# Performance work log

Measured on AMD Instinct MI355X. Metric: run time of the kernel, lower is better.

## Reference

```python
import jax, jax.numpy as jnp
import numpy as np

G_NUMS = 30      # group_nums
G_SIZE = 100     # group_size (also neighborhood_size)
BETA = 1.0
EPS = 1e-9


def setup_inputs() -> dict:
    key = jax.random.key(0)
    pointclouds = jax.random.normal(key, (8, 131072, 3), dtype=jnp.float32)
    return {"pointclouds": pointclouds}


def _knn_gather(points, queries, k):
    """points [b,N,3], queries [b,G,3] -> k nearest points per query [b,G,k,3]."""
    # squared distances [b,G,N]
    d2 = (
        jnp.sum(queries * queries, axis=-1)[..., None]
        - 2.0 * jnp.einsum("bgd,bnd->bgn", queries, points)
        + jnp.sum(points * points, axis=-1)[:, None, :]
    )
    _, idx = jax.lax.top_k(-d2, k)                    # [b,G,k]
    nbrs = jax.vmap(lambda p, i: p[i])(points, idx)   # [b,G,k,3]
    return nbrs


def reference(pointclouds):
    b, N, _ = pointclouds.shape
    # --- group_points: uniform-stride sampled centers, k-NN groups, group means ---
    stride = N // G_NUMS
    centers = pointclouds[:, ::stride][:, :G_NUMS]                 # [b,G,3]
    grouped = _knn_gather(pointclouds, centers, G_SIZE)            # [b,G,K,3]
    group_means = jnp.mean(grouped, axis=2)                        # [b,G,3]

    # --- estimate_pointcloud_local_coord_frames: per-group 3x3 PCA ---
    nbrs = _knn_gather(pointclouds, group_means, G_SIZE)           # [b,G,K,3]
    mu = jnp.mean(nbrs, axis=2, keepdims=True)
    X = nbrs - mu
    cov = jnp.einsum("bgkd,bgke->bgde", X, X) / G_SIZE             # [b,G,3,3]
    curvatures, frames = jnp.linalg.eigh(cov)                      # eigvals ascending

    # --- elongated-shape loss ---
    denom = curvatures[..., 0] + curvatures[..., 1] + curvatures[..., 2] + EPS
    first_vec = curvatures[..., 2] / denom
    second_vec = curvatures[..., 1] / denom
    elongated_shape_loss = -jnp.sum(first_vec - second_vec) / b

    # --- angular smoothness cost over group means / principal directions ---
    dirs = frames[..., :, 2]                                       # [b,G,3] largest-eig direction
    dm = jnp.sum(
        (group_means[:, :, None, :] - group_means[:, None, :, :]) ** 2, axis=-1
    )                                                              # [b,G,G]
    dm = dm + jnp.eye(G_NUMS, dtype=dm.dtype) * jnp.float32(1e30)  # exclude self
    j = jnp.argmin(dm, axis=-1)                                    # [b,G]
    dirs_j = jnp.take_along_axis(dirs, j[..., None], axis=1)       # [b,G,3]
    cos = jnp.sum(dirs * dirs_j, axis=-1)
    dlo_smooth_loss = jnp.mean(1.0 - cos * cos)                    # sign-invariant angle cost

    return elongated_shape_loss + BETA * dlo_smooth_loss
```

## Files before the change

### kernel.cpp

```cpp
#include <hip/hip_runtime.h>
#include <math.h>

#define N_PTS     131072
#define G_NUMS    30
#define G_SIZE    100
#define PT_STRIDE (N_PTS / G_NUMS)
#define TPB       1024
#define NWAVES    (TPB / 64)
#define BINS      4096
#define JB        (BINS / TPB)
#define SHIFT     20
#define SAMPLE_GRPS 1024
#define RANK_CUT  32
#define CAP       3072
#define TIE_CAP   64

struct KSmem {
    union {
        unsigned hist[BINS];
        struct {
            float gm[256][3];
            float dir[256][3];
            float pe[NWAVES];
            float ps[NWAVES];
        } fin;
    };
    unsigned wsum[NWAVES];
    unsigned T;
    int ns, nd, nt;
    unsigned u[CAP];
    int idx[CAP];
    float px[CAP], py[CAP], pz[CAP];
    int sel[G_SIZE];
    unsigned tu[TIE_CAP];
    int ti[TIE_CAP];
    float acc[3], cov[6], q[3];
    unsigned tau0, maxu, r1;
    float delta2;
};

__device__ __forceinline__ float dist2f(float px, float py, float pz,
                                        float qx, float qy, float qz) {
    float dx = px - qx, dy = py - qy, dz = pz - qz;
    return fmaf(dx, dx, fmaf(dy, dy, dz * dz));
}

__device__ __forceinline__ unsigned find_bin(KSmem& sm, unsigned rank,
                                             int tid, int lane, int wid) {
    unsigned hv[JB], csum = 0;
#pragma unroll
    for (int j = 0; j < JB; j++) { hv[j] = sm.hist[tid * JB + j]; csum += hv[j]; }
    unsigned inc = csum;
#pragma unroll
    for (int off = 1; off < 64; off <<= 1) {
        unsigned n = __shfl_up(inc, off);
        if (lane >= off) inc += n;
    }
    __syncthreads();
    if (lane == 63) sm.wsum[wid] = inc;
    __syncthreads();
    unsigned base = 0;
    for (int w = 0; w < wid; w++) base += sm.wsum[w];
    unsigned c = base + inc - csum;
#pragma unroll
    for (int j = 0; j < JB; j++) {
        if (c < rank && c + hv[j] >= rank) sm.T = (unsigned)(tid * JB + j);
        c += hv[j];
    }
    __syncthreads();
    return sm.T;
}

__device__ __forceinline__ void push4(KSmem& sm, const float4& xv, const float4& yv,
                                      const float4& zv, int i, unsigned tau,
                                      float qx, float qy, float qz) {
    unsigned u0 = __float_as_uint(dist2f(xv.x, yv.x, zv.x, qx, qy, qz));
    unsigned u1 = __float_as_uint(dist2f(xv.y, yv.y, zv.y, qx, qy, qz));
    unsigned u2 = __float_as_uint(dist2f(xv.z, yv.z, zv.z, qx, qy, qz));
    unsigned u3 = __float_as_uint(dist2f(xv.w, yv.w, zv.w, qx, qy, qz));
    int i0 = i * 4;
    if (u0 < tau) { int p = atomicAdd(&sm.ns, 1); if (p < CAP) { sm.u[p] = u0; sm.idx[p] = i0;     sm.px[p] = xv.x; sm.py[p] = yv.x; sm.pz[p] = zv.x; } }
    if (u1 < tau) { int p = atomicAdd(&sm.ns, 1); if (p < CAP) { sm.u[p] = u1; sm.idx[p] = i0 + 1; sm.px[p] = xv.y; sm.py[p] = yv.y; sm.pz[p] = zv.y; } }
    if (u2 < tau) { int p = atomicAdd(&sm.ns, 1); if (p < CAP) { sm.u[p] = u2; sm.idx[p] = i0 + 2; sm.px[p] = xv.z; sm.py[p] = yv.z; sm.pz[p] = zv.z; } }
    if (u3 < tau) { int p = atomicAdd(&sm.ns, 1); if (p < CAP) { sm.u[p] = u3; sm.idx[p] = i0 + 3; sm.px[p] = xv.w; sm.py[p] = yv.w; sm.pz[p] = zv.w; } }
}

template<bool SOA>
__device__ void knn_select(const float4* __restrict__ P4,
                           const float4* __restrict__ X4,
                           const float4* __restrict__ Y4,
                           const float4* __restrict__ Z4,
                           KSmem& sm, float qx, float qy, float qz,
                           int tid, int lane, int wid, bool save_tau) {
    for (int j = tid; j < BINS; j += TPB) sm.hist[j] = 0u;
    if (tid == 0) { sm.ns = 0; sm.nd = 0; sm.nt = 0; sm.T = 0u; }
    __syncthreads();

    if constexpr (SOA) {
        for (int i = tid; i < SAMPLE_GRPS; i += TPB) {
            float4 xv = X4[i], yv = Y4[i], zv = Z4[i];
            atomicAdd(&sm.hist[__float_as_uint(dist2f(xv.x, yv.x, zv.x, qx, qy, qz)) >> SHIFT], 1u);
            atomicAdd(&sm.hist[__float_as_uint(dist2f(xv.y, yv.y, zv.y, qx, qy, qz)) >> SHIFT], 1u);
            atomicAdd(&sm.hist[__float_as_uint(dist2f(xv.z, yv.z, zv.z, qx, qy, qz)) >> SHIFT], 1u);
            atomicAdd(&sm.hist[__float_as_uint(dist2f(xv.w, yv.w, zv.w, qx, qy, qz)) >> SHIFT], 1u);
        }
    } else {
        for (int grp = tid; grp < SAMPLE_GRPS; grp += TPB) {
            float4 f0 = P4[3 * grp + 0];
            float4 f1 = P4[3 * grp + 1];
            float4 f2 = P4[3 * grp + 2];
            atomicAdd(&sm.hist[__float_as_uint(dist2f(f0.x, f0.y, f0.z, qx, qy, qz)) >> SHIFT], 1u);
            atomicAdd(&sm.hist[__float_as_uint(dist2f(f0.w, f1.x, f1.y, qx, qy, qz)) >> SHIFT], 1u);
            atomicAdd(&sm.hist[__float_as_uint(dist2f(f1.z, f1.w, f2.x, qx, qy, qz)) >> SHIFT], 1u);
            atomicAdd(&sm.hist[__float_as_uint(dist2f(f2.y, f2.z, f2.w, qx, qy, qz)) >> SHIFT], 1u);
        }
    }
    __syncthreads();
    unsigned Tc = find_bin(sm, RANK_CUT, tid, lane, wid);
    const unsigned tau = (Tc >= BINS - 1) ? 0xFFFFFFFFu : ((Tc + 1) << SHIFT);
    if (save_tau && tid == 0) sm.tau0 = tau;
    for (int j = tid; j < BINS; j += TPB) sm.hist[j] = 0u;
    __syncthreads();

    if constexpr (SOA) {
        for (int base = 0; base < N_PTS / 4; base += TPB * 4) {
            int ia = base + tid, ib = ia + TPB, ic = ib + TPB, id_ = ic + TPB;
            float4 xa = X4[ia], ya = Y4[ia], za = Z4[ia];
            float4 xb = X4[ib], yb = Y4[ib], zb = Z4[ib];
            float4 xc = X4[ic], yc = Y4[ic], zc = Z4[ic];
            float4 xd = X4[id_], yd = Y4[id_], zd = Z4[id_];
            push4(sm, xa, ya, za, ia, tau, qx, qy, qz);
            push4(sm, xb, yb, zb, ib, tau, qx, qy, qz);
            push4(sm, xc, yc, zc, ic, tau, qx, qy, qz);
            push4(sm, xd, yd, zd, id_, tau, qx, qy, qz);
        }
    } else {
#pragma unroll 4
        for (int grp = tid; grp < N_PTS / 4; grp += TPB) {
            float4 f0 = P4[3 * grp + 0];
            float4 f1 = P4[3 * grp + 1];
            float4 f2 = P4[3 * grp + 2];
            float4 xv = make_float4(f0.x, f0.w, f1.z, f2.y);
            float4 yv = make_float4(f0.y, f1.x, f1.w, f2.z);
            float4 zv = make_float4(f0.z, f1.y, f2.x, f2.w);
            push4(sm, xv, yv, zv, grp, tau, qx, qy, qz);
        }
    }
    __syncthreads();
    int S = sm.ns; if (S > CAP) S = CAP;

    unsigned hb = 32u - (unsigned)__clz(tau - 1u);
    unsigned s2 = hb > 12u ? hb - 12u : 0u;
    for (int i = tid; i < S; i += TPB) atomicAdd(&sm.hist[sm.u[i] >> s2], 1u);
    __syncthreads();
    unsigned T2 = find_bin(sm, G_SIZE, tid, lane, wid);
    const unsigned lo = T2 << s2;

    for (int i = tid; i < S; i += TPB) {
        unsigned uu = sm.u[i];
        if (uu < lo) {
            int p = atomicAdd(&sm.nd, 1);
            if (p < G_SIZE) sm.sel[p] = i;
        } else if ((uu >> s2) == T2) {
            int p = atomicAdd(&sm.nt, 1);
            if (p < TIE_CAP) { sm.tu[p] = uu; sm.ti[p] = i; }
        }
    }
    __syncthreads();
    if (tid == 0) {
        int nd = sm.nd; if (nd > G_SIZE) nd = G_SIZE;
        int need = G_SIZE - nd;
        int ec = sm.nt; if (ec > TIE_CAP) ec = TIE_CAP;
        for (int a = 0; a < need && a < ec; ++a) {
            int best = a;
            for (int j = a + 1; j < ec; ++j)
                if (sm.tu[j] < sm.tu[best] ||
                    (sm.tu[j] == sm.tu[best] && sm.idx[sm.ti[j]] < sm.idx[sm.ti[best]])) best = j;
            unsigned tub = sm.tu[best]; sm.tu[best] = sm.tu[a]; sm.tu[a] = tub;
            int tib = sm.ti[best]; sm.ti[best] = sm.ti[a]; sm.ti[a] = tib;
            sm.sel[nd + a] = sm.ti[a];
        }
    }
    __syncthreads();
}

__device__ void eig3(const float cf[6], double lam_out[3], double dir_out[3]) {
    double a[3][3], v[3][3];
    a[0][0] = cf[0]; a[0][1] = cf[1]; a[0][2] = cf[2];
    a[1][0] = cf[1]; a[1][1] = cf[3]; a[1][2] = cf[4];
    a[2][0] = cf[2]; a[2][1] = cf[4]; a[2][2] = cf[5];
    for (int i = 0; i < 3; i++)
        for (int j = 0; j < 3; j++) v[i][j] = (i == j) ? 1.0 : 0.0;

    for (int sweep = 0; sweep < 12; sweep++) {
        double off = a[0][1] * a[0][1] + a[0][2] * a[0][2] + a[1][2] * a[1][2];
        if (off == 0.0) break;
        for (int p = 0; p < 2; p++) {
            for (int q = p + 1; q < 3; q++) {
                double apq = a[p][q];
                if (apq == 0.0) continue;
                double app = a[p][p], aqq = a[q][q];
                double theta = (aqq - app) / (2.0 * apq);
                double t = (theta >= 0.0 ? 1.0 : -1.0) /
                           (fabs(theta) + sqrt(theta * theta + 1.0));
                double c = 1.0 / sqrt(t * t + 1.0);
                double s = t * c;
                a[p][p] = app - t * apq;
                a[q][q] = aqq + t * apq;
                a[p][q] = 0.0; a[q][p] = 0.0;
                for (int r = 0; r < 3; r++) {
                    if (r == p || r == q) continue;
                    double arp = a[r][p], arq = a[r][q];
                    a[r][p] = c * arp - s * arq; a[p][r] = a[r][p];
                    a[r][q] = s * arp + c * arq; a[q][r] = a[r][q];
                }
                for (int r = 0; r < 3; r++) {
                    double vrp = v[r][p], vrq = v[r][q];
                    v[r][p] = c * vrp - s * vrq;
                    v[r][q] = s * vrp + c * vrq;
                }
            }
        }
    }
    double l0 = a[0][0], l1 = a[1][1], l2 = a[2][2];
    int i0 = 0, i1 = 1, i2 = 2;
    if (l0 > l1) { double t = l0; l0 = l1; l1 = t; int ti = i0; i0 = i1; i1 = ti; }
    if (l1 > l2) { double t = l1; l1 = l2; l2 = t; int ti = i1; i1 = i2; i2 = ti; }
    if (l0 > l1) { double t = l0; l0 = l1; l1 = t; int ti = i0; i0 = i1; i1 = ti; }
    lam_out[0] = l0; lam_out[1] = l1; lam_out[2] = l2;
    dir_out[0] = v[0][i2]; dir_out[1] = v[1][i2]; dir_out[2] = v[2][i2];
}

template<bool SOA>
__global__ __launch_bounds__(TPB)
void fused_knn_kernel(const float* __restrict__ pts,
                      const float* __restrict__ sx, const float* __restrict__ sy,
                      const float* __restrict__ sz,
                      float* __restrict__ gmeans, float* __restrict__ covs,
                      float* __restrict__ out,
                      unsigned* __restrict__ syncw,
                      int B, int nblk) {
    __shared__ KSmem sm;
    __shared__ int s_fastok;
    __shared__ int s_last;

    const int blk = blockIdx.x;
    const int b = blk % B;
    const int g = blk / B;
    const int gi = b * G_NUMS + g;
    const float* __restrict__ P = pts + (size_t)b * (N_PTS * 3);
    const float4* __restrict__ P4 = (const float4*)P;
    const float4* X4 = nullptr; const float4* Y4 = nullptr; const float4* Z4 = nullptr;
    if constexpr (SOA) {
        X4 = (const float4*)(sx + (size_t)b * N_PTS);
        Y4 = (const float4*)(sy + (size_t)b * N_PTS);
        Z4 = (const float4*)(sz + (size_t)b * N_PTS);
    }
    const int tid = threadIdx.x;
    const int lane = tid & 63, wid = tid >> 6;

    if (tid == 0) {
        const float* qp = P + (size_t)g * PT_STRIDE * 3;
        sm.q[0] = qp[0]; sm.q[1] = qp[1]; sm.q[2] = qp[2];
    }
    if (tid < 3) sm.acc[tid] = 0.f;
    if (tid < 6) sm.cov[tid] = 0.f;
    __syncthreads();
    const float qx = sm.q[0], qy = sm.q[1], qz = sm.q[2];

    knn_select<SOA>(P4, X4, Y4, Z4, sm, qx, qy, qz, tid, lane, wid, true);

    if (tid < G_SIZE) {
        int p = sm.sel[tid];
        atomicAdd(&sm.acc[0], sm.px[p]);
        atomicAdd(&sm.acc[1], sm.py[p]);
        atomicAdd(&sm.acc[2], sm.pz[p]);
    }
    __syncthreads();
    const int S0 = sm.ns;
    if (tid == 0) {
        float mx = sm.acc[0] * (1.0f / G_SIZE);
        float my = sm.acc[1] * (1.0f / G_SIZE);
        float mz = sm.acc[2] * (1.0f / G_SIZE);
        gmeans[(size_t)gi * 3 + 0] = mx;
        gmeans[(size_t)gi * 3 + 1] = my;
        gmeans[(size_t)gi * 3 + 2] = mz;
        float dx = mx - qx, dy = my - qy, dz = mz - qz;
        sm.delta2 = fmaf(dx, dx, fmaf(dy, dy, dz * dz));
        sm.q[0] = mx; sm.q[1] = my; sm.q[2] = mz;
        sm.acc[0] = 0.f; sm.acc[1] = 0.f; sm.acc[2] = 0.f;
        sm.maxu = 0u; sm.r1 = 0u; sm.T = 0u;
        sm.nd = 0; sm.nt = 0;
        s_last = 0;
        s_fastok = 0;
    }
    __syncthreads();
    const float q1x = sm.q[0], q1y = sm.q[1], q1z = sm.q[2];

    const bool attempt = (S0 >= G_SIZE) && (S0 <= CAP);
    if (attempt) {
        for (int j = tid; j < BINS; j += TPB) sm.hist[j] = 0u;
        for (int i = tid; i < S0; i += TPB) {
            unsigned uu = __float_as_uint(
                dist2f(sm.px[i], sm.py[i], sm.pz[i], q1x, q1y, q1z));
            sm.u[i] = uu;
            atomicMax(&sm.maxu, uu);
        }
        __syncthreads();
        unsigned maxu = sm.maxu;
        unsigned hb = (maxu == 0u) ? 0u : (32u - (unsigned)__clz(maxu));
        unsigned s3 = hb > 12u ? hb - 12u : 0u;
        for (int i = tid; i < S0; i += TPB) atomicAdd(&sm.hist[sm.u[i] >> s3], 1u);
        __syncthreads();
        unsigned T2 = find_bin(sm, G_SIZE, tid, lane, wid);
        const unsigned lo = T2 << s3;
        for (int i = tid; i < S0; i += TPB) {
            unsigned uu = sm.u[i];
            if (uu < lo) {
                int p = atomicAdd(&sm.nd, 1);
                if (p < G_SIZE) sm.sel[p] = i;
            } else if ((uu >> s3) == T2) {
                int p = atomicAdd(&sm.nt, 1);
                if (p < TIE_CAP) { sm.tu[p] = uu; sm.ti[p] = i; }
            }
        }
        __syncthreads();
        if (tid == 0) {
            int ok = 1;
            int nd = sm.nd; if (nd > G_SIZE) { nd = G_SIZE; ok = 0; }
            int need = G_SIZE - nd;
            if (sm.nt > TIE_CAP) ok = 0;
            int ec = sm.nt; if (ec > TIE_CAP) ec = TIE_CAP;
            if (need > ec) ok = 0;
            for (int a = 0; a < need && a < ec; ++a) {
                int best = a;
                for (int j = a + 1; j < ec; ++j)
                    if (sm.tu[j] < sm.tu[best] ||
                        (sm.tu[j] == sm.tu[best] && sm.idx[sm.ti[j]] < sm.idx[sm.ti[best]])) best = j;
                unsigned tub = sm.tu[best]; sm.tu[best] = sm.tu[a]; sm.tu[a] = tub;
                int tib = sm.ti[best]; sm.ti[best] = sm.ti[a]; sm.ti[a] = tib;
                sm.sel[nd + a] = sm.ti[a];
            }
            s_fastok = ok;
        }
        __syncthreads();
        if (s_fastok) {
            if (tid < G_SIZE) atomicMax(&sm.r1, sm.u[sm.sel[tid]]);
            __syncthreads();
            if (tid == 0) {
                double R0 = sqrt((double)__uint_as_float(sm.tau0));
                double dl = sqrt((double)sm.delta2);
                double r1 = sqrt((double)__uint_as_float(sm.r1));
                if (!((R0 - dl) > r1 * 1.0001 + 1e-7)) s_fastok = 0;
            }
            __syncthreads();
        }
    }

    if (!attempt || !s_fastok) {
        knn_select<SOA>(P4, X4, Y4, Z4, sm, q1x, q1y, q1z, tid, lane, wid, false);
    }

    float px = 0.f, py = 0.f, pz = 0.f;
    if (tid < G_SIZE) {
        int p = sm.sel[tid];
        px = sm.px[p]; py = sm.py[p]; pz = sm.pz[p];
        atomicAdd(&sm.acc[0], px);
        atomicAdd(&sm.acc[1], py);
        atomicAdd(&sm.acc[2], pz);
    }
    __syncthreads();
    float mx = sm.acc[0] * (1.0f / G_SIZE);
    float my = sm.acc[1] * (1.0f / G_SIZE);
    float mz = sm.acc[2] * (1.0f / G_SIZE);
    if (tid < G_SIZE) {
        float x = px - mx, y = py - my, z = pz - mz;
        atomicAdd(&sm.cov[0], x * x);
        atomicAdd(&sm.cov[1], x * y);
        atomicAdd(&sm.cov[2], x * z);
        atomicAdd(&sm.cov[3], y * y);
        atomicAdd(&sm.cov[4], y * z);
        atomicAdd(&sm.cov[5], z * z);
    }
    __syncthreads();
    if (tid < 6) covs[(size_t)gi * 6 + tid] = sm.cov[tid] * (1.0f / G_SIZE);

    __syncthreads();
    if (tid == 0) {
        unsigned old = __hip_atomic_fetch_add(&syncw[0], 1u, __ATOMIC_RELEASE,
                                              __HIP_MEMORY_SCOPE_AGENT);
        s_last = (old == (unsigned)(nblk - 1)) ? 1 : 0;
    }
    __syncthreads();
    if (!s_last) return;

    (void)__hip_atomic_load(&syncw[0], __ATOMIC_ACQUIRE, __HIP_MEMORY_SCOPE_AGENT);
    const int NG = nblk;
    float et = 0.f;
    if (tid < NG) {
        float cf[6];
#pragma unroll
        for (int j = 0; j < 6; j++) cf[j] = covs[tid * 6 + j];
        double lam[3], dir[3];
        eig3(cf, lam, dir);
        double denom = lam[0] + lam[1] + lam[2] + 1e-9;
        et = (float)((lam[2] - lam[1]) / denom);
        sm.fin.dir[tid][0] = (float)dir[0];
        sm.fin.dir[tid][1] = (float)dir[1];
        sm.fin.dir[tid][2] = (float)dir[2];
        sm.fin.gm[tid][0] = gmeans[tid * 3 + 0];
        sm.fin.gm[tid][1] = gmeans[tid * 3 + 1];
        sm.fin.gm[tid][2] = gmeans[tid * 3 + 2];
    }
    __syncthreads();

    float st = 0.f;
    if (tid < NG) {
        int bb = tid / G_NUMS, gg0 = tid % G_NUMS;
        float gx = sm.fin.gm[tid][0], gy = sm.fin.gm[tid][1], gz = sm.fin.gm[tid][2];
        float bd = 3.4e38f; int bj = 0;
        for (int gg = 0; gg < G_NUMS; gg++) {
            if (gg == gg0) continue;
            int o = bb * G_NUMS + gg;
            float dx = gx - sm.fin.gm[o][0];
            float dy = gy - sm.fin.gm[o][1];
            float dz = gz - sm.fin.gm[o][2];
            float d = dx * dx + dy * dy + dz * dz;
            if (d < bd) { bd = d; bj = gg; }
        }
        int o = bb * G_NUMS + bj;
        float cosv = sm.fin.dir[tid][0] * sm.fin.dir[o][0] +
                     sm.fin.dir[tid][1] * sm.fin.dir[o][1] +
                     sm.fin.dir[tid][2] * sm.fin.dir[o][2];
        st = 1.f - cosv * cosv;
    }

    float e = et, s2 = st;
#pragma unroll
    for (int off = 32; off > 0; off >>= 1) {
        e += __shfl_down(e, off);
        s2 += __shfl_down(s2, off);
    }
    if (lane == 0) { sm.fin.pe[wid] = e; sm.fin.ps[wid] = s2; }
    __syncthreads();
    if (tid == 0) {
        float se = 0.f, ss = 0.f;
        for (int w = 0; w < NWAVES; w++) { se += sm.fin.pe[w]; ss += sm.fin.ps[w]; }
        out[0] = -se / (float)B + ss / (float)NG;
    }
}

__global__ __launch_bounds__(256)
void transpose_kernel(const float* __restrict__ pts,
                      float* __restrict__ sx, float* __restrict__ sy,
                      float* __restrict__ sz, int total4) {
    int t = blockIdx.x * 256 + threadIdx.x;
    if (t >= total4) return;
    const float4* __restrict__ P4 = (const float4*)pts;
    float4 f0 = P4[3 * t + 0];
    float4 f1 = P4[3 * t + 1];
    float4 f2 = P4[3 * t + 2];
    ((float4*)sx)[t] = make_float4(f0.x, f0.w, f1.z, f2.y);
    ((float4*)sy)[t] = make_float4(f0.y, f1.x, f1.w, f2.z);
    ((float4*)sz)[t] = make_float4(f0.z, f1.y, f2.x, f2.w);
}

extern "C" void kernel_launch(void* const* d_in, const int* in_sizes, int n_in,
                              void* d_out, int out_size, void* d_ws, size_t ws_size,
                              hipStream_t stream) {
    const float* pts = (const float*)d_in[0];
    float* out = (float*)d_out;
    float* ws = (float*)d_ws;
    int B = in_sizes[0] / (N_PTS * 3);
    int nblk = B * G_NUMS;

    float* gmeans = ws;
    float* covs = ws + (size_t)B * G_NUMS * 3;
    const size_t base_floats = (size_t)B * G_NUMS * 9;
    unsigned* syncw = (unsigned*)(ws + base_floats);
    float* soa = ws + base_floats + 16;
    const size_t soa_floats = 3 * (size_t)B * N_PTS;
    const bool use_soa = ws_size >= (base_floats + 16 + soa_floats) * sizeof(float);

    hipMemsetAsync(syncw, 0, 64, stream);

    dim3 grid(nblk);
    if (use_soa) {
        float* sx = soa;
        float* sy = sx + (size_t)B * N_PTS;
        float* sz = sy + (size_t)B * N_PTS;
        int total4 = B * N_PTS / 4;
        transpose_kernel<<<dim3((total4 + 255) / 256), dim3(256), 0, stream>>>(
            pts, sx, sy, sz, total4);
        fused_knn_kernel<true><<<grid, TPB, 0, stream>>>(
            pts, sx, sy, sz, gmeans, covs, out, syncw, B, nblk);
    } else {
        fused_knn_kernel<false><<<grid, TPB, 0, stream>>>(
            pts, nullptr, nullptr, nullptr, gmeans, covs, out, syncw, B, nblk);
    }
}
```

Baseline: 140.1 us.

## Replace SoA float transpose with 8-bit quantized coordinate planes for KNN prefilter

```diff
diff --git a/kernel.cpp b/kernel.cpp
--- a/kernel.cpp
+++ b/kernel.cpp
@@ -14,6 +14,11 @@
 #define RANK_CUT  32
 #define CAP       3072
 #define TIE_CAP   64
+#define QS        0.0625f
+#define QOFF      (-8.0f + 0.03125f)
+#define QMARGIN   0.0542f
+
+typedef unsigned char uchar_t;
 
 struct KSmem {
     union {
@@ -71,6 +76,45 @@
     return sm.T;
 }
 
+__device__ void fine_select(KSmem& sm, unsigned ubound, int tid, int lane, int wid) {
+    int S = sm.ns; if (S > CAP) S = CAP;
+    unsigned hb = 32u - (unsigned)__clz(ubound | 1u);
+    unsigned s2 = hb > 12u ? hb - 12u : 0u;
+    for (int i = tid; i < S; i += TPB) {
+        unsigned bin = sm.u[i] >> s2; if (bin > BINS - 1u) bin = BINS - 1u;
+        atomicAdd(&sm.hist[bin], 1u);
+    }
+    __syncthreads();
+    unsigned T2 = find_bin(sm, G_SIZE, tid, lane, wid);
+    for (int i = tid; i < S; i += TPB) {
+        unsigned uu = sm.u[i];
+        unsigned bin = uu >> s2; if (bin > BINS - 1u) bin = BINS - 1u;
+        if (bin < T2) {
+            int p = atomicAdd(&sm.nd, 1);
+            if (p < G_SIZE) sm.sel[p] = i;
+        } else if (bin == T2) {
+            int p = atomicAdd(&sm.nt, 1);
+            if (p < TIE_CAP) { sm.tu[p] = uu; sm.ti[p] = i; }
+        }
+    }
+    __syncthreads();
+    if (tid == 0) {
+        int nd = sm.nd; if (nd > G_SIZE) nd = G_SIZE;
+        int need = G_SIZE - nd;
+        int ec = sm.nt; if (ec > TIE_CAP) ec = TIE_CAP;
+        for (int a = 0; a < need && a < ec; ++a) {
+            int best = a;
+            for (int j = a + 1; j < ec; ++j)
+                if (sm.tu[j] < sm.tu[best] ||
+                    (sm.tu[j] == sm.tu[best] && sm.idx[sm.ti[j]] < sm.idx[sm.ti[best]])) best = j;
+            unsigned tub = sm.tu[best]; sm.tu[best] = sm.tu[a]; sm.tu[a] = tub;
+            int tib = sm.ti[best]; sm.ti[best] = sm.ti[a]; sm.ti[a] = tib;
+            sm.sel[nd + a] = sm.ti[a];
+        }
+    }
+    __syncthreads();
+}
+
 __device__ __forceinline__ void push4(KSmem& sm, const float4& xv, const float4& yv,
                                       const float4& zv, int i, unsigned tau,
                                       float qx, float qy, float qz) {
@@ -85,103 +129,113 @@
     if (u3 < tau) { int p = atomicAdd(&sm.ns, 1); if (p < CAP) { sm.u[p] = u3; sm.idx[p] = i0 + 3; sm.px[p] = xv.w; sm.py[p] = yv.w; sm.pz[p] = zv.w; } }
 }
 
-template<bool SOA>
-__device__ void knn_select(const float4* __restrict__ P4,
-                           const float4* __restrict__ X4,
-                           const float4* __restrict__ Y4,
-                           const float4* __restrict__ Z4,
-                           KSmem& sm, float qx, float qy, float qz,
-                           int tid, int lane, int wid, bool save_tau) {
+__device__ void filter_exact(const float4* __restrict__ P4, KSmem& sm, unsigned tau,
+                             float qx, float qy, float qz, int tid) {
+    if (tid == 0) sm.ns = 0;
+    __syncthreads();
+#pragma unroll 4
+    for (int grp = tid; grp < N_PTS / 4; grp += TPB) {
+        float4 f0 = P4[3 * grp + 0];
+        float4 f1 = P4[3 * grp + 1];
+        float4 f2 = P4[3 * grp + 2];
+        float4 xv = make_float4(f0.x, f0.w, f1.z, f2.y);
+        float4 yv = make_float4(f0.y, f1.x, f1.w, f2.z);
+        float4 zv = make_float4(f0.z, f1.y, f2.x, f2.w);
+        push4(sm, xv, yv, zv, grp, tau, qx, qy, qz);
+    }
+    __syncthreads();
+}
+
+__device__ unsigned sample_tau(const float4* __restrict__ P4, KSmem& sm,
+                               float qx, float qy, float qz,
+                               int tid, int lane, int wid) {
     for (int j = tid; j < BINS; j += TPB) sm.hist[j] = 0u;
     if (tid == 0) { sm.ns = 0; sm.nd = 0; sm.nt = 0; sm.T = 0u; }
     __syncthreads();
-
-    if constexpr (SOA) {
-        for (int i = tid; i < SAMPLE_GRPS; i += TPB) {
-            float4 xv = X4[i], yv = Y4[i], zv = Z4[i];
-            atomicAdd(&sm.hist[__float_as_uint(dist2f(xv.x, yv.x, zv.x, qx, qy, qz)) >> SHIFT], 1u);
-            atomicAdd(&sm.hist[__float_as_uint(dist2f(xv.y, yv.y, zv.y, qx, qy, qz)) >> SHIFT], 1u);
-            atomicAdd(&sm.hist[__float_as_uint(dist2f(xv.z, yv.z, zv.z, qx, qy, qz)) >> SHIFT], 1u);
-            atomicAdd(&sm.hist[__float_as_uint(dist2f(xv.w, yv.w, zv.w, qx, qy, qz)) >> SHIFT], 1u);
-        }
-    } else {
-        for (int grp = tid; grp < SAMPLE_GRPS; grp += TPB) {
-            float4 f0 = P4[3 * grp + 0];
-            float4 f1 = P4[3 * grp + 1];
-            float4 f2 = P4[3 * grp + 2];
-            atomicAdd(&sm.hist[__float_as_uint(dist2f(f0.x, f0.y, f0.z, qx, qy, qz)) >> SHIFT], 1u);
-            atomicAdd(&sm.hist[__float_as_uint(dist2f(f0.w, f1.x, f1.y, qx, qy, qz)) >> SHIFT], 1u);
-            atomicAdd(&sm.hist[__float_as_uint(dist2f(f1.z, f1.w, f2.x, qx, qy, qz)) >> SHIFT], 1u);
-            atomicAdd(&sm.hist[__float_as_uint(dist2f(f2.y, f2.z, f2.w, qx, qy, qz)) >> SHIFT], 1u);
-        }
+    for (int grp = tid; grp < SAMPLE_GRPS; grp += TPB) {
+        float4 f0 = P4[3 * grp + 0];
+        float4 f1 = P4[3 * grp + 1];
+        float4 f2 = P4[3 * grp + 2];
+        atomicAdd(&sm.hist[__float_as_uint(dist2f(f0.x, f0.y, f0.z, qx, qy, qz)) >> SHIFT], 1u);
+        atomicAdd(&sm.hist[__float_as_uint(dist2f(f0.w, f1.x, f1.y, qx, qy, qz)) >> SHIFT], 1u);
+        atomicAdd(&sm.hist[__float_as_uint(dist2f(f1.z, f1.w, f2.x, qx, qy, qz)) >> SHIFT], 1u);
+        atomicAdd(&sm.hist[__float_as_uint(dist2f(f2.y, f2.z, f2.w, qx, qy, qz)) >> SHIFT], 1u);
     }
     __syncthreads();
     unsigned Tc = find_bin(sm, RANK_CUT, tid, lane, wid);
-    const unsigned tau = (Tc >= BINS - 1) ? 0xFFFFFFFFu : ((Tc + 1) << SHIFT);
+    unsigned tau = (Tc >= BINS - 1) ? 0xFFFFFFFFu : ((Tc + 1) << SHIFT);
+    for (int j = tid; j < BINS; j += TPB) sm.hist[j] = 0u;
+    __syncthreads();
+    return tau;
+}
+
+__device__ void knn_exact(const float4* __restrict__ P4, KSmem& sm,
+                          float qx, float qy, float qz,
+                          int tid, int lane, int wid, bool save_tau) {
+    unsigned tau = sample_tau(P4, sm, qx, qy, qz, tid, lane, wid);
     if (save_tau && tid == 0) sm.tau0 = tau;
-    for (int j = tid; j < BINS; j += TPB) sm.hist[j] = 0u;
-    __syncthreads();
-
-    if constexpr (SOA) {
-        for (int base = 0; base < N_PTS / 4; base += TPB * 4) {
-            int ia = base + tid, ib = ia + TPB, ic = ib + TPB, id_ = ic + TPB;
-            float4 xa = X4[ia], ya = Y4[ia], za = Z4[ia];
-            float4 xb = X4[ib], yb = Y4[ib], zb = Z4[ib];
-            float4 xc = X4[ic], yc = Y4[ic], zc = Z4[ic];
-            float4 xd = X4[id_], yd = Y4[id_], zd = Z4[id_];
-            push4(sm, xa, ya, za, ia, tau, qx, qy, qz);
-            push4(sm, xb, yb, zb, ib, tau, qx, qy, qz);
-            push4(sm, xc, yc, zc, ic, tau, qx, qy, qz);
-            push4(sm, xd, yd, zd, id_, tau, qx, qy, qz);
-        }
-    } else {
-#pragma unroll 4
-        for (int grp = tid; grp < N_PTS / 4; grp += TPB) {
-            float4 f0 = P4[3 * grp + 0];
-            float4 f1 = P4[3 * grp + 1];
-            float4 f2 = P4[3 * grp + 2];
-            float4 xv = make_float4(f0.x, f0.w, f1.z, f2.y);
-            float4 yv = make_float4(f0.y, f1.x, f1.w, f2.z);
-            float4 zv = make_float4(f0.z, f1.y, f2.x, f2.w);
-            push4(sm, xv, yv, zv, grp, tau, qx, qy, qz);
-        }
-    }
-    __syncthreads();
-    int S = sm.ns; if (S > CAP) S = CAP;
-
-    unsigned hb = 32u - (unsigned)__clz(tau - 1u);
-    unsigned s2 = hb > 12u ? hb - 12u : 0u;
-    for (int i = tid; i < S; i += TPB) atomicAdd(&sm.hist[sm.u[i] >> s2], 1u);
-    __syncthreads();
-    unsigned T2 = find_bin(sm, G_SIZE, tid, lane, wid);
-    const unsigned lo = T2 << s2;
-
+    filter_exact(P4, sm, tau, qx, qy, qz, tid);
+    fine_select(sm, tau, tid, lane, wid);
+}
+
+__device__ __forceinline__ void q8filt4(KSmem& sm, unsigned xw, unsigned yw,
+                                        unsigned zw, int i0, float tauf,
+                                        float Cx, float Cy, float Cz) {
+#pragma unroll
+    for (int j = 0; j < 4; ++j) {
+        float dx = fmaf((float)((xw >> (8 * j)) & 0xffu), QS, Cx);
+        float dy = fmaf((float)((yw >> (8 * j)) & 0xffu), QS, Cy);
+        float dz = fmaf((float)((zw >> (8 * j)) & 0xffu), QS, Cz);
+        float d2 = fmaf(dx, dx, fmaf(dy, dy, dz * dz));
+        if (d2 < tauf) {
+            int p = atomicAdd(&sm.ns, 1);
+            if (p < CAP) sm.idx[p] = i0 + j;
+        }
+    }
+}
+
+__device__ void knn_q8(const float* __restrict__ P, const float4* __restrict__ P4,
+                       const uint4* __restrict__ XQ, const uint4* __restrict__ YQ,
+                       const uint4* __restrict__ ZQ, KSmem& sm,
+                       float qx, float qy, float qz, int tid, int lane, int wid) {
+    unsigned tau = sample_tau(P4, sm, qx, qy, qz, tid, lane, wid);
+    if (tid == 0) { sm.tau0 = tau; sm.ns = 0; }
+    __syncthreads();
+    const bool bad_tau = (tau >= 0x7F800000u);
+    float tauf = 0.f; unsigned umax = 0u;
+    if (!bad_tau) {
+        float rt = sqrtf(__uint_as_float(tau)) + QMARGIN;
+        tauf = rt * rt;
+        float rm = sqrtf(tauf) + QMARGIN;
+        umax = __float_as_uint(fmaf(rm, rm, 1e-6f) * 1.0001f);
+
+        const float Cx = QOFF - qx, Cy = QOFF - qy, Cz = QOFF - qz;
+#pragma unroll 2
+        for (int it = 0; it < N_PTS / 16 / TPB; ++it) {
+            int i = it * TPB + tid;
+            uint4 xv = XQ[i], yv = YQ[i], zv = ZQ[i];
+            int i0 = i * 16;
+            q8filt4(sm, xv.x, yv.x, zv.x, i0 + 0,  tauf, Cx, Cy, Cz);
+            q8filt4(sm, xv.y, yv.y, zv.y, i0 + 4,  tauf, Cx, Cy, Cz);
+            q8filt4(sm, xv.z, yv.z, zv.z, i0 + 8,  tauf, Cx, Cy, Cz);
+            q8filt4(sm, xv.w, yv.w, zv.w, i0 + 12, tauf, Cx, Cy, Cz);
+        }
+        __syncthreads();
+    }
+    int S = sm.ns;
+    if (bad_tau || S > CAP) {
+        filter_exact(P4, sm, tau, qx, qy, qz, tid);
+        fine_select(sm, tau, tid, lane, wid);
+        return;
+    }
     for (int i = tid; i < S; i += TPB) {
-        unsigned uu = sm.u[i];
-        if (uu < lo) {
-            int p = atomicAdd(&sm.nd, 1);
-            if (p < G_SIZE) sm.sel[p] = i;
-        } else if ((uu >> s2) == T2) {
-            int p = atomicAdd(&sm.nt, 1);
-            if (p < TIE_CAP) { sm.tu[p] = uu; sm.ti[p] = i; }
-        }
-    }
-    __syncthreads();
-    if (tid == 0) {
-        int nd = sm.nd; if (nd > G_SIZE) nd = G_SIZE;
-        int need = G_SIZE - nd;
-        int ec = sm.nt; if (ec > TIE_CAP) ec = TIE_CAP;
-        for (int a = 0; a < need && a < ec; ++a) {
-            int best = a;
-            for (int j = a + 1; j < ec; ++j)
-                if (sm.tu[j] < sm.tu[best] ||
-                    (sm.tu[j] == sm.tu[best] && sm.idx[sm.ti[j]] < sm.idx[sm.ti[best]])) best = j;
-            unsigned tub = sm.tu[best]; sm.tu[best] = sm.tu[a]; sm.tu[a] = tub;
-            int tib = sm.ti[best]; sm.ti[best] = sm.ti[a]; sm.ti[a] = tib;
-            sm.sel[nd + a] = sm.ti[a];
-        }
-    }
-    __syncthreads();
+        const float* pp = P + 3 * (size_t)sm.idx[i];
+        float x = pp[0], y = pp[1], z = pp[2];
+        sm.px[i] = x; sm.py[i] = y; sm.pz[i] = z;
+        sm.u[i] = __float_as_uint(dist2f(x, y, z, qx, qy, qz));
+    }
+    __syncthreads();
+    fine_select(sm, umax, tid, lane, wid);
 }
 
 __device__ void eig3(const float cf[6], double lam_out[3], double dir_out[3]) {
@@ -191,7 +245,6 @@
     a[2][0] = cf[2]; a[2][1] = cf[4]; a[2][2] = cf[5];
     for (int i = 0; i < 3; i++)
         for (int j = 0; j < 3; j++) v[i][j] = (i == j) ? 1.0 : 0.0;
-
     for (int sweep = 0; sweep < 12; sweep++) {
         double off = a[0][1] * a[0][1] + a[0][2] * a[0][2] + a[1][2] * a[1][2];
         if (off == 0.0) break;
@@ -231,11 +284,11 @@
     dir_out[0] = v[0][i2]; dir_out[1] = v[1][i2]; dir_out[2] = v[2][i2];
 }
 
-template<bool SOA>
+template<int MODE>
 __global__ __launch_bounds__(TPB)
 void fused_knn_kernel(const float* __restrict__ pts,
-                      const float* __restrict__ sx, const float* __restrict__ sy,
-                      const float* __restrict__ sz,
+                      const uchar_t* __restrict__ xq, const uchar_t* __restrict__ yq,
+                      const uchar_t* __restrict__ zq,
                       float* __restrict__ gmeans, float* __restrict__ covs,
                       float* __restrict__ out,
                       unsigned* __restrict__ syncw,
@@ -243,6 +296,7 @@
     __shared__ KSmem sm;
     __shared__ int s_fastok;
     __shared__ int s_last;
+    __shared__ int s_exact;
 
     const int blk = blockIdx.x;
     const int b = blk % B;
@@ -250,11 +304,11 @@
     const int gi = b * G_NUMS + g;
     const float* __restrict__ P = pts + (size_t)b * (N_PTS * 3);
     const float4* __restrict__ P4 = (const float4*)P;
-    const float4* X4 = nullptr; const float4* Y4 = nullptr; const float4* Z4 = nullptr;
-    if constexpr (SOA) {
-        X4 = (const float4*)(sx + (size_t)b * N_PTS);
-        Y4 = (const float4*)(sy + (size_t)b * N_PTS);
-        Z4 = (const float4*)(sz + (size_t)b * N_PTS);
+    const uint4* XQ = nullptr; const uint4* YQ = nullptr; const uint4* ZQ = nullptr;
+    if (MODE == 1) {
+        XQ = (const uint4*)(xq + (size_t)b * N_PTS);
+        YQ = (const uint4*)(yq + (size_t)b * N_PTS);
+        ZQ = (const uint4*)(zq + (size_t)b * N_PTS);
     }
     const int tid = threadIdx.x;
     const int lane = tid & 63, wid = tid >> 6;
@@ -262,13 +316,15 @@
     if (tid == 0) {
         const float* qp = P + (size_t)g * PT_STRIDE * 3;
         sm.q[0] = qp[0]; sm.q[1] = qp[1]; sm.q[2] = qp[2];
+        s_exact = (MODE == 0) ? 1 : (syncw[1] ? 1 : 0);
     }
     if (tid < 3) sm.acc[tid] = 0.f;
     if (tid < 6) sm.cov[tid] = 0.f;
     __syncthreads();
     const float qx = sm.q[0], qy = sm.q[1], qz = sm.q[2];
 
-    knn_select<SOA>(P4, X4, Y4, Z4, sm, qx, qy, qz, tid, lane, wid, true);
+    if (s_exact) knn_exact(P4, sm, qx, qy, qz, tid, lane, wid, true);
+    else         knn_q8(P, P4, XQ, YQ, ZQ, sm, qx, qy, qz, tid, lane, wid);
 
     if (tid < G_SIZE) {
         int p = sm.sel[tid];
@@ -358,7 +414,7 @@
     }
 
     if (!attempt || !s_fastok) {
-        knn_select<SOA>(P4, X4, Y4, Z4, sm, q1x, q1y, q1z, tid, lane, wid, false);
+        knn_exact(P4, sm, q1x, q1y, q1z, tid, lane, wid, false);
     }
 
     float px = 0.f, py = 0.f, pz = 0.f;
@@ -435,13 +491,13 @@
         st = 1.f - cosv * cosv;
     }
 
-    float e = et, s2 = st;
+    float e = et, s2v = st;
 #pragma unroll
     for (int off = 32; off > 0; off >>= 1) {
         e += __shfl_down(e, off);
-        s2 += __shfl_down(s2, off);
-    }
-    if (lane == 0) { sm.fin.pe[wid] = e; sm.fin.ps[wid] = s2; }
+        s2v += __shfl_down(s2v, off);
+    }
+    if (lane == 0) { sm.fin.pe[wid] = e; sm.fin.ps[wid] = s2v; }
     __syncthreads();
     if (tid == 0) {
         float se = 0.f, ss = 0.f;
@@ -451,18 +507,37 @@
 }
 
 __global__ __launch_bounds__(256)
-void transpose_kernel(const float* __restrict__ pts,
-                      float* __restrict__ sx, float* __restrict__ sy,
-                      float* __restrict__ sz, int total4) {
+void quant_kernel(const float* __restrict__ pts,
+                  uchar_t* __restrict__ xq, uchar_t* __restrict__ yq,
+                  uchar_t* __restrict__ zq, unsigned* __restrict__ syncw,
+                  int total4) {
     int t = blockIdx.x * 256 + threadIdx.x;
     if (t >= total4) return;
     const float4* __restrict__ P4 = (const float4*)pts;
     float4 f0 = P4[3 * t + 0];
     float4 f1 = P4[3 * t + 1];
     float4 f2 = P4[3 * t + 2];
-    ((float4*)sx)[t] = make_float4(f0.x, f0.w, f1.z, f2.y);
-    ((float4*)sy)[t] = make_float4(f0.y, f1.x, f1.w, f2.z);
-    ((float4*)sz)[t] = make_float4(f0.z, f1.y, f2.x, f2.w);
+    float xs[4] = {f0.x, f0.w, f1.z, f2.y};
+    float ys[4] = {f0.y, f1.x, f1.w, f2.z};
+    float zs[4] = {f0.z, f1.y, f2.x, f2.w};
+    unsigned xb = 0, yb = 0, zb = 0; int bad = 0;
+#pragma unroll
+    for (int j = 0; j < 4; ++j) {
+        int ix = (int)floorf((xs[j] + 8.0f) * 16.0f);
+        int iy = (int)floorf((ys[j] + 8.0f) * 16.0f);
+        int iz = (int)floorf((zs[j] + 8.0f) * 16.0f);
+        if ((unsigned)ix > 255u || (unsigned)iy > 255u || (unsigned)iz > 255u) bad = 1;
+        ix = ix < 0 ? 0 : (ix > 255 ? 255 : ix);
+        iy = iy < 0 ? 0 : (iy > 255 ? 255 : iy);
+        iz = iz < 0 ? 0 : (iz > 255 ? 255 : iz);
+        xb |= (unsigned)ix << (8 * j);
+        yb |= (unsigned)iy << (8 * j);
+        zb |= (unsigned)iz << (8 * j);
+    }
+    ((unsigned*)xq)[t] = xb;
+    ((unsigned*)yq)[t] = yb;
+    ((unsigned*)zq)[t] = zb;
+    if (bad) atomicOr(&syncw[1], 1u);
 }
 
 extern "C" void kernel_launch(void* const* d_in, const int* in_sizes, int n_in,
@@ -475,27 +550,28 @@
     int nblk = B * G_NUMS;
 
     float* gmeans = ws;
-    float* covs = ws + (size_t)B * G_NUMS * 3;
-    const size_t base_floats = (size_t)B * G_NUMS * 9;
-    unsigned* syncw = (unsigned*)(ws + base_floats);
-    float* soa = ws + base_floats + 16;
-    const size_t soa_floats = 3 * (size_t)B * N_PTS;
-    const bool use_soa = ws_size >= (base_floats + 16 + soa_floats) * sizeof(float);
+    float* covs = ws + (size_t)3 * nblk;
+    unsigned* syncw = (unsigned*)(ws + (size_t)9 * nblk);
+    size_t plane_off = ((size_t)9 * nblk + 16) * 4;
+    plane_off = (plane_off + 15) & ~(size_t)15;
+    uchar_t* xq = (uchar_t*)d_ws + plane_off;
+    size_t planeB = (size_t)B * N_PTS;
+    uchar_t* yq = xq + planeB;
+    uchar_t* zq = yq + planeB;
+    size_t need = plane_off + 3 * planeB;
+    const int use_q = ws_size >= need;
 
     hipMemsetAsync(syncw, 0, 64, stream);
 
     dim3 grid(nblk);
-    if (use_soa) {
-        float* sx = soa;
-        float* sy = sx + (size_t)B * N_PTS;
-        float* sz = sy + (size_t)B * N_PTS;
+    if (use_q) {
         int total4 = B * N_PTS / 4;
-        transpose_kernel<<<dim3((total4 + 255) / 256), dim3(256), 0, stream>>>(
-            pts, sx, sy, sz, total4);
-        fused_knn_kernel<true><<<grid, TPB, 0, stream>>>(
-            pts, sx, sy, sz, gmeans, covs, out, syncw, B, nblk);
+        quant_kernel<<<dim3((total4 + 255) / 256), dim3(256), 0, stream>>>(
+            pts, xq, yq, zq, syncw, total4);
+        fused_knn_kernel<1><<<grid, dim3(TPB), 0, stream>>>(
+            pts, xq, yq, zq, gmeans, covs, out, syncw, B, nblk);
     } else {
-        fused_knn_kernel<false><<<grid, TPB, 0, stream>>>(
+        fused_knn_kernel<0><<<grid, dim3(TPB), 0, stream>>>(
             pts, nullptr, nullptr, nullptr, gmeans, covs, out, syncw, B, nblk);
     }
 }
```

After: 137.5 us (median of 2 runs). About the same (-1.8%).

## Drop SoA transpose kernel; pick kNN threshold by per-wave bisection on cached sample

Applied to the files above, without the earlier changes.

```diff
diff --git a/kernel.cpp b/kernel.cpp
--- a/kernel.cpp
+++ b/kernel.cpp
@@ -14,6 +14,10 @@
 #define RANK_CUT  32
 #define CAP       3072
 #define TIE_CAP   64
+#define SMP_N     2048
+#define SMP_PL    (SMP_N / 64)
+#define SMP_CUT   12
+#define SMP_ITERS 13
 
 struct KSmem {
     union {
@@ -71,6 +75,45 @@
     return sm.T;
 }
 
+__device__ void fine_select(KSmem& sm, unsigned ubound, int tid, int lane, int wid) {
+    int S = sm.ns; if (S > CAP) S = CAP;
+    unsigned hb = 32u - (unsigned)__clz(ubound | 1u);
+    unsigned s2 = hb > 12u ? hb - 12u : 0u;
+    for (int i = tid; i < S; i += TPB) {
+        unsigned bin = sm.u[i] >> s2; if (bin > BINS - 1u) bin = BINS - 1u;
+        atomicAdd(&sm.hist[bin], 1u);
+    }
+    __syncthreads();
+    unsigned T2 = find_bin(sm, G_SIZE, tid, lane, wid);
+    for (int i = tid; i < S; i += TPB) {
+        unsigned uu = sm.u[i];
+        unsigned bin = uu >> s2; if (bin > BINS - 1u) bin = BINS - 1u;
+        if (bin < T2) {
+            int p = atomicAdd(&sm.nd, 1);
+            if (p < G_SIZE) sm.sel[p] = i;
+        } else if (bin == T2) {
+            int p = atomicAdd(&sm.nt, 1);
+            if (p < TIE_CAP) { sm.tu[p] = uu; sm.ti[p] = i; }
+        }
+    }
+    __syncthreads();
+    if (tid == 0) {
+        int nd = sm.nd; if (nd > G_SIZE) nd = G_SIZE;
+        int need = G_SIZE - nd;
+        int ec = sm.nt; if (ec > TIE_CAP) ec = TIE_CAP;
+        for (int a = 0; a < need && a < ec; ++a) {
+            int best = a;
+            for (int j = a + 1; j < ec; ++j)
+                if (sm.tu[j] < sm.tu[best] ||
+                    (sm.tu[j] == sm.tu[best] && sm.idx[sm.ti[j]] < sm.idx[sm.ti[best]])) best = j;
+            unsigned tub = sm.tu[best]; sm.tu[best] = sm.tu[a]; sm.tu[a] = tub;
+            int tib = sm.ti[best]; sm.ti[best] = sm.ti[a]; sm.ti[a] = tib;
+            sm.sel[nd + a] = sm.ti[a];
+        }
+    }
+    __syncthreads();
+}
+
 __device__ __forceinline__ void push4(KSmem& sm, const float4& xv, const float4& yv,
                                       const float4& zv, int i, unsigned tau,
                                       float qx, float qy, float qz) {
@@ -85,103 +128,53 @@
     if (u3 < tau) { int p = atomicAdd(&sm.ns, 1); if (p < CAP) { sm.u[p] = u3; sm.idx[p] = i0 + 3; sm.px[p] = xv.w; sm.py[p] = yv.w; sm.pz[p] = zv.w; } }
 }
 
-template<bool SOA>
-__device__ void knn_select(const float4* __restrict__ P4,
-                           const float4* __restrict__ X4,
-                           const float4* __restrict__ Y4,
-                           const float4* __restrict__ Z4,
-                           KSmem& sm, float qx, float qy, float qz,
-                           int tid, int lane, int wid, bool save_tau) {
+__device__ void filter_exact(const float4* __restrict__ P4, KSmem& sm, unsigned tau,
+                             float qx, float qy, float qz, int tid) {
+    if (tid == 0) sm.ns = 0;
+    __syncthreads();
+#pragma unroll 4
+    for (int grp = tid; grp < N_PTS / 4; grp += TPB) {
+        float4 f0 = P4[3 * grp + 0];
+        float4 f1 = P4[3 * grp + 1];
+        float4 f2 = P4[3 * grp + 2];
+        float4 xv = make_float4(f0.x, f0.w, f1.z, f2.y);
+        float4 yv = make_float4(f0.y, f1.x, f1.w, f2.z);
+        float4 zv = make_float4(f0.z, f1.y, f2.x, f2.w);
+        push4(sm, xv, yv, zv, grp, tau, qx, qy, qz);
+    }
+    __syncthreads();
+}
+
+__device__ unsigned sample_tau(const float4* __restrict__ P4, KSmem& sm,
+                               float qx, float qy, float qz,
+                               int tid, int lane, int wid) {
     for (int j = tid; j < BINS; j += TPB) sm.hist[j] = 0u;
     if (tid == 0) { sm.ns = 0; sm.nd = 0; sm.nt = 0; sm.T = 0u; }
     __syncthreads();
-
-    if constexpr (SOA) {
-        for (int i = tid; i < SAMPLE_GRPS; i += TPB) {
-            float4 xv = X4[i], yv = Y4[i], zv = Z4[i];
-            atomicAdd(&sm.hist[__float_as_uint(dist2f(xv.x, yv.x, zv.x, qx, qy, qz)) >> SHIFT], 1u);
-            atomicAdd(&sm.hist[__float_as_uint(dist2f(xv.y, yv.y, zv.y, qx, qy, qz)) >> SHIFT], 1u);
-            atomicAdd(&sm.hist[__float_as_uint(dist2f(xv.z, yv.z, zv.z, qx, qy, qz)) >> SHIFT], 1u);
-            atomicAdd(&sm.hist[__float_as_uint(dist2f(xv.w, yv.w, zv.w, qx, qy, qz)) >> SHIFT], 1u);
-        }
-    } else {
-        for (int grp = tid; grp < SAMPLE_GRPS; grp += TPB) {
-            float4 f0 = P4[3 * grp + 0];
-            float4 f1 = P4[3 * grp + 1];
-            float4 f2 = P4[3 * grp + 2];
-            atomicAdd(&sm.hist[__float_as_uint(dist2f(f0.x, f0.y, f0.z, qx, qy, qz)) >> SHIFT], 1u);
-            atomicAdd(&sm.hist[__float_as_uint(dist2f(f0.w, f1.x, f1.y, qx, qy, qz)) >> SHIFT], 1u);
-            atomicAdd(&sm.hist[__float_as_uint(dist2f(f1.z, f1.w, f2.x, qx, qy, qz)) >> SHIFT], 1u);
-            atomicAdd(&sm.hist[__float_as_uint(dist2f(f2.y, f2.z, f2.w, qx, qy, qz)) >> SHIFT], 1u);
-        }
+    for (int grp = tid; grp < SAMPLE_GRPS; grp += TPB) {
+        float4 f0 = P4[3 * grp + 0];
+        float4 f1 = P4[3 * grp + 1];
+        float4 f2 = P4[3 * grp + 2];
+        atomicAdd(&sm.hist[__float_as_uint(dist2f(f0.x, f0.y, f0.z, qx, qy, qz)) >> SHIFT], 1u);
+        atomicAdd(&sm.hist[__float_as_uint(dist2f(f0.w, f1.x, f1.y, qx, qy, qz)) >> SHIFT], 1u);
+        atomicAdd(&sm.hist[__float_as_uint(dist2f(f1.z, f1.w, f2.x, qx, qy, qz)) >> SHIFT], 1u);
+        atomicAdd(&sm.hist[__float_as_uint(dist2f(f2.y, f2.z, f2.w, qx, qy, qz)) >> SHIFT], 1u);
     }
     __syncthreads();
     unsigned Tc = find_bin(sm, RANK_CUT, tid, lane, wid);
-    const unsigned tau = (Tc >= BINS - 1) ? 0xFFFFFFFFu : ((Tc + 1) << SHIFT);
+    unsigned tau = (Tc >= BINS - 1) ? 0xFFFFFFFFu : ((Tc + 1) << SHIFT);
+    for (int j = tid; j < BINS; j += TPB) sm.hist[j] = 0u;
+    __syncthreads();
+    return tau;
+}
+
+__device__ void knn_exact(const float4* __restrict__ P4, KSmem& sm,
+                          float qx, float qy, float qz,
+                          int tid, int lane, int wid, bool save_tau) {
+    unsigned tau = sample_tau(P4, sm, qx, qy, qz, tid, lane, wid);
     if (save_tau && tid == 0) sm.tau0 = tau;
-    for (int j = tid; j < BINS; j += TPB) sm.hist[j] = 0u;
-    __syncthreads();
-
-    if constexpr (SOA) {
-        for (int base = 0; base < N_PTS / 4; base += TPB * 4) {
-            int ia = base + tid, ib = ia + TPB, ic = ib + TPB, id_ = ic + TPB;
-            float4 xa = X4[ia], ya = Y4[ia], za = Z4[ia];
-            float4 xb = X4[ib], yb = Y4[ib], zb = Z4[ib];
-            float4 xc = X4[ic], yc = Y4[ic], zc = Z4[ic];
-            float4 xd = X4[id_], yd = Y4[id_], zd = Z4[id_];
-            push4(sm, xa, ya, za, ia, tau, qx, qy, qz);
-            push4(sm, xb, yb, zb, ib, tau, qx, qy, qz);
-            push4(sm, xc, yc, zc, ic, tau, qx, qy, qz);
-            push4(sm, xd, yd, zd, id_, tau, qx, qy, qz);
-        }
-    } else {
-#pragma unroll 4
-        for (int grp = tid; grp < N_PTS / 4; grp += TPB) {
-            float4 f0 = P4[3 * grp + 0];
-            float4 f1 = P4[3 * grp + 1];
-            float4 f2 = P4[3 * grp + 2];
-            float4 xv = make_float4(f0.x, f0.w, f1.z, f2.y);
-            float4 yv = make_float4(f0.y, f1.x, f1.w, f2.z);
-            float4 zv = make_float4(f0.z, f1.y, f2.x, f2.w);
-            push4(sm, xv, yv, zv, grp, tau, qx, qy, qz);
-        }
-    }
-    __syncthreads();
-    int S = sm.ns; if (S > CAP) S = CAP;
-
-    unsigned hb = 32u - (unsigned)__clz(tau - 1u);
-    unsigned s2 = hb > 12u ? hb - 12u : 0u;
-    for (int i = tid; i < S; i += TPB) atomicAdd(&sm.hist[sm.u[i] >> s2], 1u);
-    __syncthreads();
-    unsigned T2 = find_bin(sm, G_SIZE, tid, lane, wid);
-    const unsigned lo = T2 << s2;
-
-    for (int i = tid; i < S; i += TPB) {
-        unsigned uu = sm.u[i];
-        if (uu < lo) {
-            int p = atomicAdd(&sm.nd, 1);
-            if (p < G_SIZE) sm.sel[p] = i;
-        } else if ((uu >> s2) == T2) {
-            int p = atomicAdd(&sm.nt, 1);
-            if (p < TIE_CAP) { sm.tu[p] = uu; sm.ti[p] = i; }
-        }
-    }
-    __syncthreads();
-    if (tid == 0) {
-        int nd = sm.nd; if (nd > G_SIZE) nd = G_SIZE;
-        int need = G_SIZE - nd;
-        int ec = sm.nt; if (ec > TIE_CAP) ec = TIE_CAP;
-        for (int a = 0; a < need && a < ec; ++a) {
-            int best = a;
-            for (int j = a + 1; j < ec; ++j)
-                if (sm.tu[j] < sm.tu[best] ||
-                    (sm.tu[j] == sm.tu[best] && sm.idx[sm.ti[j]] < sm.idx[sm.ti[best]])) best = j;
-            unsigned tub = sm.tu[best]; sm.tu[best] = sm.tu[a]; sm.tu[a] = tub;
-            int tib = sm.ti[best]; sm.ti[best] = sm.ti[a]; sm.ti[a] = tib;
-            sm.sel[nd + a] = sm.ti[a];
-        }
-    }
-    __syncthreads();
+    filter_exact(P4, sm, tau, qx, qy, qz, tid);
+    fine_select(sm, tau, tid, lane, wid);
 }
 
 __device__ void eig3(const float cf[6], double lam_out[3], double dir_out[3]) {
@@ -191,7 +184,6 @@
     a[2][0] = cf[2]; a[2][1] = cf[4]; a[2][2] = cf[5];
     for (int i = 0; i < 3; i++)
         for (int j = 0; j < 3; j++) v[i][j] = (i == j) ? 1.0 : 0.0;
-
     for (int sweep = 0; sweep < 12; sweep++) {
         double off = a[0][1] * a[0][1] + a[0][2] * a[0][2] + a[1][2] * a[1][2];
         if (off == 0.0) break;
@@ -231,11 +223,8 @@
     dir_out[0] = v[0][i2]; dir_out[1] = v[1][i2]; dir_out[2] = v[2][i2];
 }
 
-template<bool SOA>
 __global__ __launch_bounds__(TPB)
 void fused_knn_kernel(const float* __restrict__ pts,
-                      const float* __restrict__ sx, const float* __restrict__ sy,
-                      const float* __restrict__ sz,
                       float* __restrict__ gmeans, float* __restrict__ covs,
                       float* __restrict__ out,
                       unsigned* __restrict__ syncw,
@@ -250,25 +239,63 @@
     const int gi = b * G_NUMS + g;
     const float* __restrict__ P = pts + (size_t)b * (N_PTS * 3);
     const float4* __restrict__ P4 = (const float4*)P;
-    const float4* X4 = nullptr; const float4* Y4 = nullptr; const float4* Z4 = nullptr;
-    if constexpr (SOA) {
-        X4 = (const float4*)(sx + (size_t)b * N_PTS);
-        Y4 = (const float4*)(sy + (size_t)b * N_PTS);
-        Z4 = (const float4*)(sz + (size_t)b * N_PTS);
-    }
     const int tid = threadIdx.x;
     const int lane = tid & 63, wid = tid >> 6;
 
     if (tid == 0) {
         const float* qp = P + (size_t)g * PT_STRIDE * 3;
         sm.q[0] = qp[0]; sm.q[1] = qp[1]; sm.q[2] = qp[2];
+        sm.ns = 0; sm.nd = 0; sm.nt = 0; sm.T = 0u;
+        s_last = 0;
     }
     if (tid < 3) sm.acc[tid] = 0.f;
     if (tid < 6) sm.cov[tid] = 0.f;
+    for (int j = tid; j < BINS; j += TPB) sm.hist[j] = 0u;
+    for (int t = tid; t < SMP_N / 4; t += TPB) {
+        float4 f0 = P4[3 * t + 0];
+        float4 f1 = P4[3 * t + 1];
+        float4 f2 = P4[3 * t + 2];
+        sm.px[4 * t + 0] = f0.x; sm.px[4 * t + 1] = f0.w;
+        sm.px[4 * t + 2] = f1.z; sm.px[4 * t + 3] = f2.y;
+        sm.py[4 * t + 0] = f0.y; sm.py[4 * t + 1] = f1.x;
+        sm.py[4 * t + 2] = f1.w; sm.py[4 * t + 3] = f2.z;
+        sm.pz[4 * t + 0] = f0.z; sm.pz[4 * t + 1] = f1.y;
+        sm.pz[4 * t + 2] = f2.x; sm.pz[4 * t + 3] = f2.w;
+    }
     __syncthreads();
     const float qx = sm.q[0], qy = sm.q[1], qz = sm.q[2];
 
-    knn_select<SOA>(P4, X4, Y4, Z4, sm, qx, qy, qz, tid, lane, wid, true);
+    unsigned tau;
+    {
+        unsigned du[SMP_PL];
+#pragma unroll
+        for (int k = 0; k < SMP_PL; ++k) {
+            int p = lane + 64 * k;
+            du[k] = __float_as_uint(dist2f(sm.px[p], sm.py[p], sm.pz[p], qx, qy, qz));
+        }
+        unsigned lo = 0u, hi = 0x7F800000u;
+        for (int it = 0; it < SMP_ITERS; ++it) {
+            unsigned mid = (lo + hi) >> 1;
+            int cnt = 0;
+#pragma unroll
+            for (int k = 0; k < SMP_PL; ++k) cnt += (du[k] < mid) ? 1 : 0;
+#pragma unroll
+            for (int off = 1; off < 64; off <<= 1) cnt += __shfl_xor(cnt, off);
+            if (cnt >= SMP_CUT) hi = mid; else lo = mid;
+        }
+        tau = hi;
+    }
+    __syncthreads();
+    if (tid == 0) sm.tau0 = tau;
+
+    filter_exact(P4, sm, tau, qx, qy, qz, tid);
+    int S0 = sm.ns;
+    bool anomaly = (S0 < G_SIZE) || (S0 > CAP);
+    if (anomaly) {
+        knn_exact(P4, sm, qx, qy, qz, tid, lane, wid, true);
+    } else {
+        fine_select(sm, tau, tid, lane, wid);
+    }
 
     if (tid < G_SIZE) {
         int p = sm.sel[tid];
@@ -277,7 +304,7 @@
         atomicAdd(&sm.acc[2], sm.pz[p]);
     }
     __syncthreads();
-    const int S0 = sm.ns;
+    S0 = sm.ns;
     if (tid == 0) {
         float mx = sm.acc[0] * (1.0f / G_SIZE);
         float my = sm.acc[1] * (1.0f / G_SIZE);
@@ -291,7 +318,6 @@
         sm.acc[0] = 0.f; sm.acc[1] = 0.f; sm.acc[2] = 0.f;
         sm.maxu = 0u; sm.r1 = 0u; sm.T = 0u;
         sm.nd = 0; sm.nt = 0;
-        s_last = 0;
         s_fastok = 0;
     }
     __syncthreads();
@@ -358,7 +384,7 @@
     }
 
     if (!attempt || !s_fastok) {
-        knn_select<SOA>(P4, X4, Y4, Z4, sm, q1x, q1y, q1z, tid, lane, wid, false);
+        knn_exact(P4, sm, q1x, q1y, q1z, tid, lane, wid, false);
     }
 
     float px = 0.f, py = 0.f, pz = 0.f;
@@ -435,34 +461,19 @@
         st = 1.f - cosv * cosv;
     }
 
-    float e = et, s2 = st;
+    float e = et, s2v = st;
 #pragma unroll
     for (int off = 32; off > 0; off >>= 1) {
         e += __shfl_down(e, off);
-        s2 += __shfl_down(s2, off);
-    }
-    if (lane == 0) { sm.fin.pe[wid] = e; sm.fin.ps[wid] = s2; }
+        s2v += __shfl_down(s2v, off);
+    }
+    if (lane == 0) { sm.fin.pe[wid] = e; sm.fin.ps[wid] = s2v; }
     __syncthreads();
     if (tid == 0) {
         float se = 0.f, ss = 0.f;
         for (int w = 0; w < NWAVES; w++) { se += sm.fin.pe[w]; ss += sm.fin.ps[w]; }
         out[0] = -se / (float)B + ss / (float)NG;
     }
-}
-
-__global__ __launch_bounds__(256)
-void transpose_kernel(const float* __restrict__ pts,
-                      float* __restrict__ sx, float* __restrict__ sy,
-                      float* __restrict__ sz, int total4) {
-    int t = blockIdx.x * 256 + threadIdx.x;
-    if (t >= total4) return;
-    const float4* __restrict__ P4 = (const float4*)pts;
-    float4 f0 = P4[3 * t + 0];
-    float4 f1 = P4[3 * t + 1];
-    float4 f2 = P4[3 * t + 2];
-    ((float4*)sx)[t] = make_float4(f0.x, f0.w, f1.z, f2.y);
-    ((float4*)sy)[t] = make_float4(f0.y, f1.x, f1.w, f2.z);
-    ((float4*)sz)[t] = make_float4(f0.z, f1.y, f2.x, f2.w);
 }
 
 extern "C" void kernel_launch(void* const* d_in, const int* in_sizes, int n_in,
@@ -475,27 +486,11 @@
     int nblk = B * G_NUMS;
 
     float* gmeans = ws;
-    float* covs = ws + (size_t)B * G_NUMS * 3;
-    const size_t base_floats = (size_t)B * G_NUMS * 9;
-    unsigned* syncw = (unsigned*)(ws + base_floats);
-    float* soa = ws + base_floats + 16;
-    const size_t soa_floats = 3 * (size_t)B * N_PTS;
-    const bool use_soa = ws_size >= (base_floats + 16 + soa_floats) * sizeof(float);
+    float* covs = ws + (size_t)3 * nblk;
+    unsigned* syncw = (unsigned*)(ws + (size_t)9 * nblk);
 
     hipMemsetAsync(syncw, 0, 64, stream);
 
-    dim3 grid(nblk);
-    if (use_soa) {
-        float* sx = soa;
-        float* sy = sx + (size_t)B * N_PTS;
-        float* sz = sy + (size_t)B * N_PTS;
-        int total4 = B * N_PTS / 4;
-        transpose_kernel<<<dim3((total4 + 255) / 256), dim3(256), 0, stream>>>(
-            pts, sx, sy, sz, total4);
-        fused_knn_kernel<true><<<grid, TPB, 0, stream>>>(
-            pts, sx, sy, sz, gmeans, covs, out, syncw, B, nblk);
-    } else {
-        fused_knn_kernel<false><<<grid, TPB, 0, stream>>>(
-            pts, nullptr, nullptr, nullptr, gmeans, covs, out, syncw, B, nblk);
-    }
-}
+    fused_knn_kernel<<<dim3(nblk), dim3(TPB), 0, stream>>>(
+        pts, gmeans, covs, out, syncw, B, nblk);
+}
```

Measured after the change: 146.8 us. 4.8% more time.
